# Optimization experiments

Measured on AMD Instinct MI355X. Metric: run time of the kernel, lower is better.

Reference implementation:

```python
import jax, jax.numpy as jnp
import numpy as np

B, S, F_IN, H, F_OUT, BB = 128, 1024, 128, 256, 128, 256


def setup_inputs() -> dict:
    key = jax.random.key(0)
    ks = jax.random.split(key, 16)
    s_in = 1.0 / np.sqrt(F_IN + H)
    s_bb = 1.0 / np.sqrt(BB)
    s_h = 1.0 / np.sqrt(H)
    return {
        "x": jax.random.normal(ks[0], (B, S, F_IN), dtype=jnp.float32),
        "ts": jax.random.uniform(ks[1], (B, S), dtype=jnp.float32),
        # backbone (depth=1): Linear(F_IN+H -> BB)
        "Wb": jax.random.normal(ks[2], (F_IN + H, BB), dtype=jnp.float32) * s_in,
        "bb": jnp.zeros((BB,), jnp.float32),
        # CfC heads: ff1, ff2, time_a, time_b (BB -> H)
        "Wff1": jax.random.normal(ks[3], (BB, H), dtype=jnp.float32) * s_bb,
        "bff1": jnp.zeros((H,), jnp.float32),
        "Wff2": jax.random.normal(ks[4], (BB, H), dtype=jnp.float32) * s_bb,
        "bff2": jnp.zeros((H,), jnp.float32),
        "Wta": jax.random.normal(ks[5], (BB, H), dtype=jnp.float32) * s_bb,
        "bta": jnp.zeros((H,), jnp.float32),
        "Wtb": jax.random.normal(ks[6], (BB, H), dtype=jnp.float32) * s_bb,
        "btb": jnp.zeros((H,), jnp.float32),
        # output projection Linear(H -> F_OUT)
        "Wout": jax.random.normal(ks[7], (H, F_OUT), dtype=jnp.float32) * s_h,
        "bout": jnp.zeros((F_OUT,), jnp.float32),
    }


def reference(x, ts, Wb, bb, Wff1, bff1, Wff2, bff2, Wta, bta, Wtb, btb, Wout, bout):
    # x: [B,S,F_IN], ts: [B,S] -> out: [B,S,F_OUT]
    batch = x.shape[0]
    hidden = Wff1.shape[1]

    def step(h, inp):
        xt, tt = inp  # xt: [B,F_IN], tt: [B]
        z = jnp.tanh(jnp.concatenate([xt, h], axis=-1) @ Wb + bb)  # backbone [B,BB]
        ff1 = jnp.tanh(z @ Wff1 + bff1)
        ff2 = jnp.tanh(z @ Wff2 + bff2)
        t_a = z @ Wta + bta
        t_b = z @ Wtb + btb
        t_interp = jax.nn.sigmoid(t_a * tt[:, None] + t_b)  # time-dependent gate
        h_new = ff1 * (1.0 - t_interp) + t_interp * ff2
        y = h_new @ Wout + bout
        return h_new, y

    h0 = jnp.zeros((batch, hidden), dtype=x.dtype)
    xs = (jnp.swapaxes(x, 0, 1), jnp.swapaxes(ts, 0, 1))  # time-major for scan
    _, ys = jax.lax.scan(step, h0, xs)  # ys: [S,B,F_OUT]
    return jnp.swapaxes(ys, 0, 1)
```

## Files before the change

### kernel.cpp

```cpp
#include <hip/hip_runtime.h>

#define Bn   128
#define Sn   1024
#define FIN  128
#define Hn   256
#define FOUT 128
#define KBB  384
#define NT1  1024

#define NV 12
#define NL 8
#define DYN_SMEM (NL * 1024 * 8 * 2)

#define WB_OFF 0
#define W4_OFF 98304
#define WO_OFF 360448
#define WS_HALVES 393216
#define HBUF_OFF WS_HALVES
#define WS_SPLIT_BYTES ((size_t)(WS_HALVES + (size_t)Bn * Sn * Hn) * 2)

typedef _Float16 h2 __attribute__((ext_vector_type(2)));
typedef _Float16 h8 __attribute__((ext_vector_type(8)));

__device__ __forceinline__ float dot2f(h2 a, h2 b, float c) {
#if __has_builtin(__builtin_amdgcn_fdot2)
  return __builtin_amdgcn_fdot2(a, b, c, false);
#else
  return c + (float)a[0] * (float)b[0] + (float)a[1] * (float)b[1];
#endif
}
__device__ __forceinline__ void dot8_4(h8 v, h8 w, float& c0, float& c1, float& c2, float& c3) {
  h2 v0 = {v[0], v[1]}, v1 = {v[2], v[3]}, v2 = {v[4], v[5]}, v3 = {v[6], v[7]};
  h2 w0 = {w[0], w[1]}, w1 = {w[2], w[3]}, w2 = {w[4], w[5]}, w3 = {w[6], w[7]};
  c0 = dot2f(v0, w0, c0); c1 = dot2f(v1, w1, c1);
  c2 = dot2f(v2, w2, c2); c3 = dot2f(v3, w3, c3);
}

__global__ __launch_bounds__(256) void pack_w(
    const float* __restrict__ Wb, const float* __restrict__ W1,
    const float* __restrict__ W2, const float* __restrict__ W3,
    const float* __restrict__ W4, const float* __restrict__ Wo,
    _Float16* __restrict__ ws) {
  int p = blockIdx.x * 256 + threadIdx.x;
  if (p >= WS_HALVES) return;
  float v;
  if (p < W4_OFF) {
    int r = p & 7, j = (p >> 3) & 255;
    int k = ((p >> 11) << 3) | r;
    v = Wb[k * 256 + j];
  } else if (p < WO_OFF) {
    int q = p - W4_OFF;
    int r = q & 7, j = (q >> 3) & 1023;
    int k = ((q >> 13) << 3) | r;
    int jj = j & 255;
    const float* Ws = (j < 256) ? W1 : (j < 512) ? W2 : (j < 768) ? W3 : W4;
    v = Ws[k * 256 + jj];
  } else {
    int q = p - WO_OFF;
    int r = q & 7, j = (q >> 3) & 127;
    int k = ((q >> 10) << 3) | r;
    v = Wo[k * 128 + j];
  }
  ws[p] = (_Float16)v;
}

template <int INLINE_Y>
__global__ __launch_bounds__(NT1, 4) void cfc3(
    const float* __restrict__ x, const float* __restrict__ ts,
    const float* __restrict__ bb, const float* __restrict__ bf1,
    const float* __restrict__ bf2, const float* __restrict__ bta,
    const float* __restrict__ btb, const float* __restrict__ bo,
    _Float16* __restrict__ ws, float* __restrict__ out) {
  __shared__ __align__(16) _Float16 xh[KBB];
  __shared__ __align__(16) _Float16 zf[Hn];
  __shared__ float tsb[Sn];
  __shared__ float scrZ[768];
  __shared__ float scrH[768];
  __shared__ float scrY[896];
  extern __shared__ _Float16 sWH[];

  const int tid = threadIdx.x;
  const int b = blockIdx.x;
  const _Float16* Wb_p = ws + WB_OFF;
  const _Float16* W4_p = ws + W4_OFF;
  const _Float16* Wo_p = ws + WO_OFF;
  _Float16* hbuf = ws + HBUF_OFF;

  const float* xrow  = x  + (size_t)b * Sn * FIN;
  const float* tsrow = ts + (size_t)b * Sn;
  float*       orow  = out + (size_t)b * Sn * FOUT;

  const int jq = tid & 255;
  const int kw = tid >> 8;
  const float bbj = (tid < 256) ? bb[tid] : 0.f;
  const float bH = (kw == 0 ? bf1 : kw == 1 ? bf2 : kw == 2 ? bta : btb)[jq];
  const int jY = tid & 127, kq = tid >> 7;
  const float boj = (tid < 128) ? bo[tid] : 0.f;

  const _Float16* gZ = Wb_p + ((size_t)(kw * 12) * 256 + jq) * 8;
  const _Float16* gH = W4_p + (size_t)tid * 8;
  const _Float16* gY = Wo_p + ((size_t)(kq * 4) * 128 + jY) * 8;

  h8 wH[NV];
#pragma unroll
  for (int c = 0; c < NV; ++c) wH[c] = *(const h8*)(gH + (size_t)c * 8192);
#pragma unroll
  for (int c = 0; c < NV; ++c) asm volatile("" : "+v"(wH[c]));
#pragma unroll
  for (int cc = 0; cc < NL; ++cc)
    *(h8*)(sWH + (size_t)cc * 8192 + tid * 8) =
        *(const h8*)(gH + (size_t)(NV + cc) * 8192);

  tsb[tid] = tsrow[tid];
  if (tid < 128) ((unsigned*)xh)[64 + tid] = 0;
  if (tid < 64) {
    float2 xv = *(const float2*)(xrow + 2 * tid);
    h2 p; p[0] = (_Float16)xv.x; p[1] = (_Float16)xv.y;
    *(h2*)&xh[2 * tid] = p;
  }
  __syncthreads();

  for (int st = 0; st < Sn; ++st) {
    float2 xv; xv.x = 0.f; xv.y = 0.f;
    if (tid >= 960 && st + 1 < Sn)
      xv = *(const float2*)(xrow + (size_t)(st + 1) * FIN + 2 * (tid - 960));

    float a0 = 0.f, a1 = 0.f, a2 = 0.f, a3 = 0.f;
#pragma unroll 4
    for (int c = 0; c < 12; ++c) {
      h8 v = *(const h8*)&xh[(kw * 12 + c) * 8];
      h8 w = *(const h8*)(gZ + (size_t)c * 2048);
      dot8_4(v, w, a0, a1, a2, a3);
    }
    float zs = a0 + a1 + a2 + a3;
    if (tid >= 256) scrZ[tid - 256] = zs;
    __syncthreads();
    if (tid < 256) {
      float zp = zs + scrZ[tid] + scrZ[256 + tid] + scrZ[512 + tid] + bbj;
      zf[tid] = (_Float16)tanhf(zp);
    }
    if (tid >= 960 && st + 1 < Sn) {
      h2 p; p[0] = (_Float16)xv.x; p[1] = (_Float16)xv.y;
      *(h2*)&xh[2 * (tid - 960)] = p;
    }
    __syncthreads();

    float b0 = 0.f, b1 = 0.f, b2 = 0.f, b3 = 0.f;
    float s0 = 0.f, s1 = 0.f, s2 = 0.f, s3 = 0.f;
#pragma unroll 4
    for (int c = NV + NL; c < 32; ++c) {
      h8 v = *(const h8*)&zf[c * 8];
      h8 w = *(const h8*)(gH + (size_t)c * 8192);
      dot8_4(v, w, s0, s1, s2, s3);
    }
#pragma unroll
    for (int c = 0; c < NV; ++c) {
      h8 v = *(const h8*)&zf[c * 8];
      dot8_4(v, wH[c], b0, b1, b2, b3);
    }
#pragma unroll
    for (int cc = 0; cc < NL; ++cc) {
      h8 v = *(const h8*)&zf[(NV + cc) * 8];
      h8 w = *(const h8*)(sWH + (size_t)cc * 8192 + tid * 8);
      dot8_4(v, w, b0, b1, b2, b3);
    }
    float g = (b0 + s0) + (b1 + s1) + (b2 + s2) + (b3 + s3) + bH;
    if (tid >= 256) scrH[tid - 256] = g;
    __syncthreads();
    if (tid < 256) {
      float ff2 = scrH[tid], ta = scrH[256 + tid], tb = scrH[512 + tid];
      float tt = tsb[st];
      float sg = 1.f / (1.f + __expf(-(ta * tt + tb)));
      float hn = tanhf(g) * (1.f - sg) + sg * tanhf(ff2);
      xh[128 + tid] = (_Float16)hn;
      if (!INLINE_Y)
        hbuf[((size_t)b * Sn + st) * Hn + tid] = (_Float16)hn;
    }
    __syncthreads();

    if (INLINE_Y) {
      float y0 = 0.f, y1 = 0.f, y2 = 0.f, y3 = 0.f;
#pragma unroll
      for (int c = 0; c < 4; ++c) {
        h8 v = *(const h8*)&xh[128 + (kq * 4 + c) * 8];
        h8 w = *(const h8*)(gY + (size_t)c * 1024);
        dot8_4(v, w, y0, y1, y2, y3);
      }
      float ys = y0 + y1 + y2 + y3;
      if (tid >= 128) scrY[tid - 128] = ys;
      __syncthreads();
      if (tid < 128) {
        float y = ys + boj;
#pragma unroll
        for (int p = 0; p < 7; ++p) y += scrY[128 * p + tid];
        orow[(size_t)st * FOUT + tid] = y;
      }
    }
  }
}

#define SMEMY (65536 + 4096)
extern "C" __global__ __launch_bounds__(256, 4)
void ygemm(const _Float16* __restrict__ ws, const float* __restrict__ bo,
           float* __restrict__ out) {
  extern __shared__ char ysm[];
  _Float16* sWo = (_Float16*)ysm;
  _Float16* sH  = (_Float16*)(ysm + 65536);
  const int tid = threadIdx.x;
  { const uint4* g = (const uint4*)(ws + WO_OFF);
    uint4* l = (uint4*)sWo;
#pragma unroll
    for (int i = 0; i < 16; ++i) l[tid + 256 * i] = g[tid + 256 * i]; }
  const _Float16* hb = ws + HBUF_OFF;
  const int row0 = blockIdx.x * 256;
  const int j = tid & 127, rh = tid >> 7;
  const float boj = bo[j];
  for (int it = 0; it < 32; ++it) {
    const int rbase = row0 + it * 8;
    __syncthreads();
    ((uint4*)sH)[tid] = ((const uint4*)(hb + (size_t)rbase * 256))[tid];
    __syncthreads();
#pragma unroll
    for (int rr = rh; rr < 8; rr += 2) {
      float y0 = 0.f, y1 = 0.f, y2 = 0.f, y3 = 0.f;
#pragma unroll 4
      for (int c = 0; c < 32; ++c) {
        h8 v = *(const h8*)&sH[rr * 256 + c * 8];
        h8 w = *(const h8*)&sWo[((size_t)c * 128 + j) * 8];
        dot8_4(v, w, y0, y1, y2, y3);
      }
      out[(size_t)(rbase + rr) * 128 + j] = y0 + y1 + y2 + y3 + boj;
    }
  }
}

extern "C" void kernel_launch(void* const* d_in, const int* in_sizes, int n_in,
                              void* d_out, int out_size, void* d_ws, size_t ws_size,
                              hipStream_t stream) {
  const float* x   = (const float*)d_in[0];
  const float* ts  = (const float*)d_in[1];
  const float* Wb  = (const float*)d_in[2];
  const float* bb  = (const float*)d_in[3];
  const float* W1  = (const float*)d_in[4];
  const float* bf1 = (const float*)d_in[5];
  const float* W2  = (const float*)d_in[6];
  const float* bf2 = (const float*)d_in[7];
  const float* W3  = (const float*)d_in[8];
  const float* bta = (const float*)d_in[9];
  const float* W4  = (const float*)d_in[10];
  const float* btb = (const float*)d_in[11];
  const float* Wo  = (const float*)d_in[12];
  const float* bo  = (const float*)d_in[13];
  float* out = (float*)d_out;
  _Float16* ws = (_Float16*)d_ws;

  pack_w<<<WS_HALVES / 256, 256, 0, stream>>>(Wb, W1, W2, W3, W4, Wo, ws);

  if (ws_size >= WS_SPLIT_BYTES) {
    hipFuncSetAttribute((const void*)(cfc3<0>),
                        hipFuncAttributeMaxDynamicSharedMemorySize, DYN_SMEM);
    cfc3<0><<<Bn, NT1, DYN_SMEM, stream>>>(x, ts, bb, bf1, bf2, bta, btb, bo, ws, out);
    hipFuncSetAttribute((const void*)ygemm,
                        hipFuncAttributeMaxDynamicSharedMemorySize, SMEMY);
    ygemm<<<(Bn * Sn) / 256, 256, SMEMY, stream>>>(ws, bo, out);
  } else {
    hipFuncSetAttribute((const void*)(cfc3<1>),
                        hipFuncAttributeMaxDynamicSharedMemorySize, DYN_SMEM);
    cfc3<1><<<Bn, NT1, DYN_SMEM, stream>>>(x, ts, bb, bf1, bf2, bta, btb, bo, ws, out);
  }
}
```

Before: 4.845 ms.

## Precompute input projection x@Wb_x in a separate GEMM before the recurrence

Adds an xgemm kernel that computes the x-part of the backbone projection for all timesteps up front and stores it as fp16 in the workspace. The recurrent kernel then does only the hidden-state part (256 of 384 K) per step and adds the precomputed value, removing per-step x loads and a third of the backbone dot work from the serial critical path. The register/LDS split of the head weights also changes (NV 12->8, NL 8->9). In exchange it needs a larger workspace, an extra pass over x, fp16 rounding of the precomputed term, and more dependent global-load latency in each step.

Result: slower. 4.972 ms (+2.6%).

```diff
diff --git a/kernel.cpp b/kernel.cpp
--- a/kernel.cpp
+++ b/kernel.cpp
@@ -8,8 +8,8 @@
 #define KBB  384
 #define NT1  1024
 
-#define NV 12
-#define NL 8
+#define NV 8
+#define NL 9
 #define DYN_SMEM (NL * 1024 * 8 * 2)
 
 #define WB_OFF 0
@@ -17,7 +17,9 @@
 #define WO_OFF 360448
 #define WS_HALVES 393216
 #define HBUF_OFF WS_HALVES
+#define XC_OFF (HBUF_OFF + (size_t)Bn * Sn * Hn)
 #define WS_SPLIT_BYTES ((size_t)(WS_HALVES + (size_t)Bn * Sn * Hn) * 2)
+#define WS_FULL_BYTES ((XC_OFF + (size_t)Bn * Sn * Hn) * 2)
 
 typedef _Float16 h2 __attribute__((ext_vector_type(2)));
 typedef _Float16 h8 __attribute__((ext_vector_type(8)));
@@ -64,7 +66,33 @@
   ws[p] = (_Float16)v;
 }
 
-template <int INLINE_Y>
+__global__ __launch_bounds__(256) void xgemm(
+    const float* __restrict__ x, const _Float16* __restrict__ ws,
+    _Float16* __restrict__ xc) {
+  __shared__ __align__(16) _Float16 sX[64 * 128];
+  const int tid = threadIdx.x;
+  const size_t r0 = (size_t)blockIdx.x * 64;
+  const float* xb = x + r0 * 128;
+#pragma unroll
+  for (int m = 0; m < 32; ++m)
+    sX[m * 256 + tid] = (_Float16)xb[m * 256 + tid];
+  const _Float16* gX = ws + WB_OFF + (size_t)tid * 8;
+  h8 wx[16];
+#pragma unroll
+  for (int L = 0; L < 16; ++L) wx[L] = *(const h8*)(gX + (size_t)L * 2048);
+  __syncthreads();
+  for (int r = 0; r < 64; ++r) {
+    float c0 = 0.f, c1 = 0.f, c2 = 0.f, c3 = 0.f;
+#pragma unroll
+    for (int L = 0; L < 16; ++L) {
+      h8 v = *(const h8*)&sX[r * 128 + L * 8];
+      dot8_4(v, wx[L], c0, c1, c2, c3);
+    }
+    xc[(r0 + r) * 256 + tid] = (_Float16)(c0 + c1 + c2 + c3);
+  }
+}
+
+template <int XC, int INLINE_Y>
 __global__ __launch_bounds__(NT1, 4) void cfc3(
     const float* __restrict__ x, const float* __restrict__ ts,
     const float* __restrict__ bb, const float* __restrict__ bf1,
@@ -85,6 +113,7 @@
   const _Float16* W4_p = ws + W4_OFF;
   const _Float16* Wo_p = ws + WO_OFF;
   _Float16* hbuf = ws + HBUF_OFF;
+  const _Float16* xcp = ws + XC_OFF;
 
   const float* xrow  = x  + (size_t)b * Sn * FIN;
   const float* tsrow = ts + (size_t)b * Sn;
@@ -97,7 +126,9 @@
   const int jY = tid & 127, kq = tid >> 7;
   const float boj = (tid < 128) ? bo[tid] : 0.f;
 
-  const _Float16* gZ = Wb_p + ((size_t)(kw * 12) * 256 + jq) * 8;
+  const _Float16* gZ = XC
+      ? Wb_p + (size_t)(16 + kw * 8) * 2048 + (size_t)jq * 8
+      : Wb_p + (size_t)(kw * 12) * 2048 + (size_t)jq * 8;
   const _Float16* gH = W4_p + (size_t)tid * 8;
   const _Float16* gY = Wo_p + ((size_t)(kq * 4) * 128 + jY) * 8;
 
@@ -113,7 +144,7 @@
 
   tsb[tid] = tsrow[tid];
   if (tid < 128) ((unsigned*)xh)[64 + tid] = 0;
-  if (tid < 64) {
+  if (XC == 0 && tid < 64) {
     float2 xv = *(const float2*)(xrow + 2 * tid);
     h2 p; p[0] = (_Float16)xv.x; p[1] = (_Float16)xv.y;
     *(h2*)&xh[2 * tid] = p;
@@ -121,38 +152,52 @@
   __syncthreads();
 
   for (int st = 0; st < Sn; ++st) {
+    float xcv = 0.f;
+    if (XC && tid < 256)
+      xcv = (float)xcp[((size_t)b * Sn + st) * 256 + tid];
+
     float2 xv; xv.x = 0.f; xv.y = 0.f;
-    if (tid >= 960 && st + 1 < Sn)
+    if (XC == 0 && tid >= 960 && st + 1 < Sn)
       xv = *(const float2*)(xrow + (size_t)(st + 1) * FIN + 2 * (tid - 960));
 
     float a0 = 0.f, a1 = 0.f, a2 = 0.f, a3 = 0.f;
+    if (XC) {
 #pragma unroll 4
-    for (int c = 0; c < 12; ++c) {
-      h8 v = *(const h8*)&xh[(kw * 12 + c) * 8];
-      h8 w = *(const h8*)(gZ + (size_t)c * 2048);
-      dot8_4(v, w, a0, a1, a2, a3);
+      for (int c = 0; c < 8; ++c) {
+        h8 v = *(const h8*)&xh[128 + (kw * 8 + c) * 8];
+        h8 w = *(const h8*)(gZ + (size_t)c * 2048);
+        dot8_4(v, w, a0, a1, a2, a3);
+      }
+    } else {
+#pragma unroll 4
+      for (int c = 0; c < 12; ++c) {
+        h8 v = *(const h8*)&xh[(kw * 12 + c) * 8];
+        h8 w = *(const h8*)(gZ + (size_t)c * 2048);
+        dot8_4(v, w, a0, a1, a2, a3);
+      }
     }
     float zs = a0 + a1 + a2 + a3;
     if (tid >= 256) scrZ[tid - 256] = zs;
     __syncthreads();
     if (tid < 256) {
       float zp = zs + scrZ[tid] + scrZ[256 + tid] + scrZ[512 + tid] + bbj;
+      if (XC) zp += xcv;
       zf[tid] = (_Float16)tanhf(zp);
     }
-    if (tid >= 960 && st + 1 < Sn) {
+    if (XC == 0 && tid >= 960 && st + 1 < Sn) {
       h2 p; p[0] = (_Float16)xv.x; p[1] = (_Float16)xv.y;
       *(h2*)&xh[2 * (tid - 960)] = p;
     }
     __syncthreads();
 
-    float b0 = 0.f, b1 = 0.f, b2 = 0.f, b3 = 0.f;
     float s0 = 0.f, s1 = 0.f, s2 = 0.f, s3 = 0.f;
-#pragma unroll 4
+#pragma unroll 2
     for (int c = NV + NL; c < 32; ++c) {
       h8 v = *(const h8*)&zf[c * 8];
       h8 w = *(const h8*)(gH + (size_t)c * 8192);
       dot8_4(v, w, s0, s1, s2, s3);
     }
+    float b0 = 0.f, b1 = 0.f, b2 = 0.f, b3 = 0.f;
 #pragma unroll
     for (int c = 0; c < NV; ++c) {
       h8 v = *(const h8*)&zf[c * 8];
@@ -256,16 +301,24 @@
 
   pack_w<<<WS_HALVES / 256, 256, 0, stream>>>(Wb, W1, W2, W3, W4, Wo, ws);
 
-  if (ws_size >= WS_SPLIT_BYTES) {
-    hipFuncSetAttribute((const void*)(cfc3<0>),
+  if (ws_size >= WS_FULL_BYTES) {
+    xgemm<<<(Bn * Sn) / 64, 256, 0, stream>>>(x, ws, ws + XC_OFF);
+    hipFuncSetAttribute((const void*)(cfc3<1, 0>),
                         hipFuncAttributeMaxDynamicSharedMemorySize, DYN_SMEM);
-    cfc3<0><<<Bn, NT1, DYN_SMEM, stream>>>(x, ts, bb, bf1, bf2, bta, btb, bo, ws, out);
+    cfc3<1, 0><<<Bn, NT1, DYN_SMEM, stream>>>(x, ts, bb, bf1, bf2, bta, btb, bo, ws, out);
+    hipFuncSetAttribute((const void*)ygemm,
+                        hipFuncAttributeMaxDynamicSharedMemorySize, SMEMY);
+    ygemm<<<(Bn * Sn) / 256, 256, SMEMY, stream>>>(ws, bo, out);
+  } else if (ws_size >= WS_SPLIT_BYTES) {
+    hipFuncSetAttribute((const void*)(cfc3<0, 0>),
+                        hipFuncAttributeMaxDynamicSharedMemorySize, DYN_SMEM);
+    cfc3<0, 0><<<Bn, NT1, DYN_SMEM, stream>>>(x, ts, bb, bf1, bf2, bta, btb, bo, ws, out);
     hipFuncSetAttribute((const void*)ygemm,
                         hipFuncAttributeMaxDynamicSharedMemorySize, SMEMY);
     ygemm<<<(Bn * Sn) / 256, 256, SMEMY, stream>>>(ws, bo, out);
   } else {
-    hipFuncSetAttribute((const void*)(cfc3<1>),
+    hipFuncSetAttribute((const void*)(cfc3<0, 1>),
                         hipFuncAttributeMaxDynamicSharedMemorySize, DYN_SMEM);
-    cfc3<1><<<Bn, NT1, DYN_SMEM, stream>>>(x, ts, bb, bf1, bf2, bta, btb, bo, ws, out);
-  }
-}
+    cfc3<0, 1><<<Bn, NT1, DYN_SMEM, stream>>>(x, ts, bb, bf1, bf2, bta, btb, bo, ws, out);
+  }
+}
```
